# Performance work log

Measured on AMD Instinct MI355X. Metric: run time of the kernel, lower is better.

The kernel has to match this reference:

```python
import jax, jax.numpy as jnp
import numpy as np
import math

B, L, DIM, H = 1, 2048, 512, 8
D = DIM // H
STEPS = 1024
TWO_PI = 2.0 * math.pi
CHUNK = 64  # matches torch chunk_size


def setup_inputs() -> dict:
    key = jax.random.key(0)
    ks = jax.random.split(key, 6)
    x = jax.random.normal(ks[0], (B, L, DIM), jnp.float32)
    W_qs = jax.random.normal(ks[1], (DIM, 2 * DIM), jnp.float32) * 0.02
    b_qs = jnp.zeros((2 * DIM,), jnp.float32)
    ln_w = jnp.ones((2 * DIM,), jnp.float32)
    ln_b = jnp.zeros((2 * DIM,), jnp.float32)
    freq = jax.random.normal(ks[2], (H,), jnp.float32) * 0.02
    phase_shift = jax.random.normal(ks[3], (H,), jnp.float32) * 0.02
    W_out = jax.random.normal(ks[4], (DIM, DIM), jnp.float32) * 0.02
    b_out = jnp.zeros((DIM,), jnp.float32)
    # buffer: cos(linspace(0, 2pi, 1024)) exactly as in _init_lookup_tables
    cos_table = jnp.cos(jnp.linspace(0.0, TWO_PI, STEPS)).astype(jnp.float32)
    return dict(x=x, W_qs=W_qs, b_qs=b_qs, ln_w=ln_w, ln_b=ln_b,
                freq=freq, phase_shift=phase_shift, W_out=W_out, b_out=b_out,
                cos_table=cos_table)


def _forward(x, W_qs, b_qs, ln_w, ln_b, freq, phase_shift, W_out, b_out, cos_table):
    # quantum state preparation (shared module applied to same x => q == k states)
    qs = x @ W_qs + b_qs                                  # [B,L,2*DIM]
    mu = jnp.mean(qs, axis=-1, keepdims=True)
    var = jnp.var(qs, axis=-1, keepdims=True)
    qs = (qs - mu) / jnp.sqrt(var + 1e-5) * ln_w + ln_b    # LayerNorm(2*dim)
    amp, phase = jnp.split(qs, 2, axis=-1)                 # [B,L,DIM] each
    amp = jax.nn.sigmoid(amp)
    amp = amp / (jnp.sqrt(jnp.sum(amp ** 2, axis=-1, keepdims=True)) + 1e-8)
    phase = jnp.tanh(phase) * math.pi

    to_heads = lambda t: t.reshape(B, L, H, D).transpose(0, 2, 1, 3)  # [B,H,L,D]
    q_amp = to_heads(amp)
    q_phase = to_heads(phase)
    v = to_heads(x)

    NC = L // CHUNK
    qa_c = q_amp.reshape(B, H, NC, CHUNK, D).transpose(2, 0, 1, 3, 4)   # [NC,B,H,C,D]
    qp_c = q_phase.reshape(B, H, NC, CHUNK, D).transpose(2, 0, 1, 3, 4)
    f = freq[None, :, None, None, None]
    s = phase_shift[None, :, None, None, None]

    def chunk(carry, qc):
        qa, qp = qc                                         # [B,H,C,D]
        # pairwise per-dim phase interference via lookup table
        pd = (qp[:, :, :, None, :] - q_phase[:, :, None, :, :]) * f + s  # [B,H,C,L,D]
        idx = ((pd / TWO_PI * STEPS) % STEPS).astype(jnp.int32)
        interf = cos_table[idx]
        score = jnp.sum(qa[:, :, :, None, :] * q_amp[:, :, None, :, :] * interf,
                        axis=-1)                            # [B,H,C,L]
        return carry, score

    _, scores = jax.lax.scan(jax.checkpoint(chunk), 0, (qa_c, qp_c))
    scores = scores.transpose(1, 2, 0, 3, 4).reshape(B, H, L, L)
    attn = jax.nn.softmax(scores / math.sqrt(D), axis=-1)
    out = jnp.einsum('bhqk,bhkd->bhqd', attn, v)            # [B,H,L,D]
    out = out.transpose(0, 2, 1, 3).reshape(B, L, DIM)
    return out @ W_out + b_out


def reference(x, W_qs, b_qs, ln_w, ln_b, freq, phase_shift, W_out, b_out, cos_table):
    return _forward(x, W_qs, b_qs, ln_w, ln_b, freq, phase_shift, W_out, b_out, cos_table)
```

## Files before the change

### kernel.cpp

```cpp
#include <hip/hip_runtime.h>
#include <cstdint>
#include <cstddef>


typedef __attribute__((ext_vector_type(8))) short short8;
typedef __attribute__((ext_vector_type(4))) float f32x4;

#define MFMA16(a, b, c) __builtin_amdgcn_mfma_f32_16x16x32_bf16((a), (b), (c), 0, 0, 0)

static constexpr size_t B_ATTB = 0;
static constexpr size_t B_UB   = (size_t)2 * 1024 * 1024;
static constexpr size_t B_WB   = B_UB + (size_t)4 * 1024 * 1024;
static constexpr size_t B_VT   = B_WB + (size_t)4 * 1024 * 1024;
static constexpr size_t B_WQT  = B_VT + (size_t)2 * 1024 * 1024;
static constexpr size_t B_WOT  = B_WQT + (size_t)1 * 1024 * 1024;

__device__ __forceinline__ unsigned short f2bf(float f) {
  unsigned u = __float_as_uint(f);
  return (unsigned short)((u + 0x7FFFu + ((u >> 16) & 1u)) >> 16);
}

__global__ __launch_bounds__(256) void k_prep(const float* __restrict__ x,
    const float* __restrict__ Wq, const float* __restrict__ Wo,
    unsigned short* __restrict__ vT, unsigned short* __restrict__ WqTp,
    unsigned short* __restrict__ WoT) {
  __shared__ float tl[64 * 65];
  const int t = threadIdx.x, b = blockIdx.x;
  if (b < 256) {
    const int i0 = (b >> 3) * 64, h = b & 7;
    #pragma unroll
    for (int it = 0; it < 16; ++it) {
      int n = t + 256 * it;
      int r = n >> 6, c = n & 63;
      tl[r * 65 + c] = x[(size_t)(i0 + r) * 512 + h * 64 + c];
    }
    __syncthreads();
    #pragma unroll
    for (int it = 0; it < 16; ++it) {
      int n = t + 256 * it;
      int d = n >> 6, ii = n & 63;
      vT[(size_t)(h * 64 + d) * 2048 + i0 + ii] = f2bf(tl[ii * 65 + d]);
    }
  } else if (b < 384) {
    const int bb = b - 256;
    const int k0 = (bb >> 4) * 64, n0 = (bb & 15) * 64;
    #pragma unroll
    for (int it = 0; it < 16; ++it) {
      int n = t + 256 * it;
      int r = n >> 6, c = n & 63;
      tl[r * 65 + c] = Wq[(size_t)(k0 + r) * 1024 + n0 + c];
    }
    __syncthreads();
    #pragma unroll
    for (int it = 0; it < 16; ++it) {
      int n = t + 256 * it;
      int rr = n >> 6, cc = n & 63;
      int nn = n0 + rr, kk = k0 + cc;
      int nt = nn >> 4, mm = nn & 15;
      int kc32 = kk >> 5, qd = (kk >> 3) & 3, j = kk & 7;
      WqTp[(((size_t)nt * 16 + kc32) * 64 + qd * 16 + mm) * 8 + j] =
          f2bf(tl[cc * 65 + rr]);
    }
  } else {
    const int bb = b - 384;
    const int k0 = (bb >> 3) * 64, n0 = (bb & 7) * 64;
    #pragma unroll
    for (int it = 0; it < 16; ++it) {
      int n = t + 256 * it;
      int r = n >> 6, c = n & 63;
      tl[r * 65 + c] = Wo[(size_t)(k0 + r) * 512 + n0 + c];
    }
    __syncthreads();
    #pragma unroll
    for (int it = 0; it < 16; ++it) {
      int n = t + 256 * it;
      int rr = n >> 6, cc = n & 63;
      WoT[(size_t)(n0 + rr) * 512 + k0 + cc] = f2bf(tl[cc * 65 + rr]);
    }
  }
}

__global__ __launch_bounds__(512) void k_qs_ln(const float* __restrict__ x,
    const unsigned short* __restrict__ WqTp, const float* __restrict__ bq,
    const float* __restrict__ lnw, const float* __restrict__ lnb,
    const float* __restrict__ fr, const float* __restrict__ psh,
    unsigned short* __restrict__ Ub, unsigned short* __restrict__ Wb) {
  __shared__ __align__(16) unsigned short s_a[16 * 520];
  __shared__ float s_amp[16 * 516];
  __shared__ float red[8 * 16 * 2];
  __shared__ float red2[4 * 16];
  const int r0 = blockIdx.x * 16, t = threadIdx.x;
  const int w = t >> 6, lane = t & 63, m = lane & 15, quad = lane >> 4;
  {
    const int row = t >> 5, cs = (t & 31) * 16;
    const float4* xr = (const float4*)(x + (size_t)(r0 + row) * 512 + cs);
    unsigned short tmp[16];
    #pragma unroll
    for (int q4 = 0; q4 < 4; ++q4) {
      float4 v = xr[q4];
      tmp[q4 * 4 + 0] = f2bf(v.x); tmp[q4 * 4 + 1] = f2bf(v.y);
      tmp[q4 * 4 + 2] = f2bf(v.z); tmp[q4 * 4 + 3] = f2bf(v.w);
    }
    *(short8*)(s_a + row * 520 + cs)     = *(short8*)(tmp);
    *(short8*)(s_a + row * 520 + cs + 8) = *(short8*)(tmp + 8);
  }
  __syncthreads();
  f32x4 acc[8] = {{0,0,0,0},{0,0,0,0},{0,0,0,0},{0,0,0,0},
                  {0,0,0,0},{0,0,0,0},{0,0,0,0},{0,0,0,0}};
  for (int kc32 = 0; kc32 < 16; ++kc32) {
    short8 af = *(const short8*)(s_a + m * 520 + kc32 * 32 + quad * 8);
    const unsigned short* bp =
        WqTp + (((size_t)(w * 8) * 16 + kc32) * 64 + lane) * 8;
    #pragma unroll
    for (int nt = 0; nt < 8; ++nt) {
      short8 bf = *(const short8*)(bp + (size_t)nt * 8192);
      acc[nt] = MFMA16(af, bf, acc[nt]);
    }
  }
  #pragma unroll
  for (int nt = 0; nt < 8; ++nt) {
    float bv = bq[w * 128 + nt * 16 + m];
    #pragma unroll
    for (int r = 0; r < 4; ++r) acc[nt][r] += bv;
  }
  float s1[4] = {0, 0, 0, 0}, s2[4] = {0, 0, 0, 0};
  #pragma unroll
  for (int r = 0; r < 4; ++r)
    #pragma unroll
    for (int nt = 0; nt < 8; ++nt) {
      float v = acc[nt][r];
      s1[r] += v; s2[r] += v * v;
    }
  #pragma unroll
  for (int off = 1; off < 16; off <<= 1)
    #pragma unroll
    for (int r = 0; r < 4; ++r) {
      s1[r] += __shfl_xor(s1[r], off, 64);
      s2[r] += __shfl_xor(s2[r], off, 64);
    }
  if (m == 0)
    #pragma unroll
    for (int r = 0; r < 4; ++r) {
      red[(w * 16 + quad * 4 + r) * 2]     = s1[r];
      red[(w * 16 + quad * 4 + r) * 2 + 1] = s2[r];
    }
  __syncthreads();
  float mu[4], rstd[4];
  #pragma unroll
  for (int r = 0; r < 4; ++r) {
    int row = quad * 4 + r;
    float S = 0, S2 = 0;
    #pragma unroll
    for (int wp = 0; wp < 8; ++wp) {
      S  += red[(wp * 16 + row) * 2];
      S2 += red[(wp * 16 + row) * 2 + 1];
    }
    mu[r] = S * (1.0f / 1024.0f);
    float var = S2 * (1.0f / 1024.0f) - mu[r] * mu[r];
    rstd[r] = 1.0f / sqrtf(var + 1e-5f);
  }
  float y[8][4];
  #pragma unroll
  for (int nt = 0; nt < 8; ++nt) {
    int c = w * 128 + nt * 16 + m;
    float gw = lnw[c], gb = lnb[c];
    #pragma unroll
    for (int r = 0; r < 4; ++r)
      y[nt][r] = (acc[nt][r] - mu[r]) * rstd[r] * gw + gb;
  }
  const float PI_F = 3.14159265358979323846f;
  if (w < 4) {
    float a[8][4];
    float na[4] = {0, 0, 0, 0};
    #pragma unroll
    for (int nt = 0; nt < 8; ++nt)
      #pragma unroll
      for (int r = 0; r < 4; ++r) {
        float v = __builtin_amdgcn_rcpf(1.0f + __expf(-y[nt][r]));
        a[nt][r] = v;
        na[r] += v * v;
      }
    #pragma unroll
    for (int off = 1; off < 16; off <<= 1)
      #pragma unroll
      for (int r = 0; r < 4; ++r) na[r] += __shfl_xor(na[r], off, 64);
    if (m == 0)
      #pragma unroll
      for (int r = 0; r < 4; ++r) red2[w * 16 + quad * 4 + r] = na[r];
    __syncthreads();
    float inv[4];
    #pragma unroll
    for (int r = 0; r < 4; ++r) {
      int row = quad * 4 + r;
      float N = red2[row] + red2[16 + row] + red2[32 + row] + red2[48 + row];
      inv[r] = 1.0f / (sqrtf(N) + 1e-8f);
    }
    #pragma unroll
    for (int nt = 0; nt < 8; ++nt)
      #pragma unroll
      for (int r = 0; r < 4; ++r)
        s_amp[(quad * 4 + r) * 516 + w * 128 + nt * 16 + m] = a[nt][r] * inv[r];
    __syncthreads();
  } else {
    float p[8][4];
    #pragma unroll
    for (int nt = 0; nt < 8; ++nt)
      #pragma unroll
      for (int r = 0; r < 4; ++r) {
        float e2 = __expf(2.0f * y[nt][r]);
        p[nt][r] = (1.0f - 2.0f * __builtin_amdgcn_rcpf(e2 + 1.0f)) * PI_F;
      }
    __syncthreads();
    __syncthreads();
    const double GAM = 1024.0 / 1023.0;
    const int hbase = (w - 4) * 2;
    float c1[2], s1g[2];
    #pragma unroll
    for (int hh = 0; hh < 2; ++hh) {
      c1[hh]  = (float)((double)fr[hbase + hh] * GAM);
      s1g[hh] = (float)((double)psh[hbase + hh] * GAM);
    }
    #pragma unroll
    for (int nt = 0; nt < 8; ++nt) {
      const int hh = nt >> 2;
      const int pc = (w - 4) * 128 + nt * 16 + m;
      const int d = pc & 63;
      #pragma unroll
      for (int r = 0; r < 4; ++r) {
        const int i = r0 + quad * 4 + r;
        float af = s_amp[(quad * 4 + r) * 516 + pc];
        float A = fmaf(p[nt][r], c1[hh], s1g[hh]);
        float Bp = p[nt][r] * c1[hh];
        float cA, sA, cB, sB;
        __sincosf(A, &sA, &cA);
        __sincosf(Bp, &sB, &cB);
        size_t base = ((size_t)(hbase + hh) * 2048 + i) * 128 + d;
        Ub[base]      = f2bf(af * cA);
        Ub[base + 64] = f2bf(af * sA);
        Wb[base]      = f2bf(af * cB);
        Wb[base + 64] = f2bf(af * sB);
      }
    }
  }
}

__global__ __launch_bounds__(512, 1) void k_flash6(const unsigned short* __restrict__ Ub,
    const unsigned short* __restrict__ Wb, const unsigned short* __restrict__ vT,
    unsigned short* __restrict__ attb) {
  __shared__ __align__(16) unsigned char s_w[2][128 * 272];
  __shared__ __align__(16) unsigned char s_v[2][64 * 272];
  __shared__ __align__(16) unsigned char s_p[2][64 * 272];
  const int qt = blockIdx.x, h = blockIdx.y;
  const int q0 = qt * 64;
  const int t = threadIdx.x;
  const int wave = t >> 6, lane = t & 63;
  const int qg = wave & 3, dh = wave >> 2;
  const int m = lane & 15, quad = lane >> 4;
  const int sr = t >> 2, sp = t & 3;
  const int vr = t >> 3, vp = t & 7;
  short8 afr[4][4];
  #pragma unroll
  for (int g = 0; g < 4; ++g) {
    const unsigned short* urow = Ub + ((size_t)h * 2048 + q0 + g * 16 + m) * 128;
    #pragma unroll
    for (int fs = 0; fs < 4; ++fs)
      afr[g][fs] = *(const short8*)(urow + fs * 32 + quad * 8);
  }
  short8 ones;
  #pragma unroll
  for (int j = 0; j < 8; ++j) ones[j] = (short)0x3F80;
  f32x4 oacc[2] = {{0,0,0,0},{0,0,0,0}};
  f32x4 dacc = {0, 0, 0, 0};
  const unsigned short* wgbase = Wb + (size_t)h * 2048 * 128 + (size_t)sr * 128;
  const unsigned short* vgbase = vT + ((size_t)h * 64 + vr) * 2048;
  #pragma unroll
  for (int it = 0; it < 4; ++it)
    *(short8*)(s_w[0] + sr * 272 + sp * 64 + it * 16) =
      *(const short8*)(wgbase + sp * 32 + it * 8);
  #pragma unroll
  for (int it = 0; it < 2; ++it)
    *(short8*)(s_v[0] + vr * 272 + vp * 32 + it * 16) =
      *(const short8*)(vgbase + vp * 16 + it * 8);
  __syncthreads();
  for (int kt = 0; kt < 16; ++kt) {
    const int cur = kt & 1;
    short8 wst[4], vst[2];
    const bool has = (kt < 15);
    if (has) {
      const unsigned short* wg = wgbase + (size_t)(kt + 1) * 128 * 128;
      #pragma unroll
      for (int it = 0; it < 4; ++it)
        wst[it] = *(const short8*)(wg + sp * 32 + it * 8);
      const unsigned short* vg = vgbase + (kt + 1) * 128;
      #pragma unroll
      for (int it = 0; it < 2; ++it)
        vst[it] = *(const short8*)(vg + vp * 16 + it * 8);
    }
    f32x4 sc[4] = {{0,0,0,0},{0,0,0,0},{0,0,0,0},{0,0,0,0}};
    #pragma unroll
    for (int fs = 0; fs < 4; ++fs) {
      short8 bfr = *(const short8*)(s_w[cur] + (wave * 16 + m) * 272 + fs * 64 + quad * 16);
      #pragma unroll
      for (int g = 0; g < 4; ++g)
        sc[g] = MFMA16(afr[g][fs], bfr, sc[g]);
    }
    #pragma unroll
    for (int g = 0; g < 4; ++g)
      #pragma unroll
      for (int r = 0; r < 4; ++r) {
        float p = __expf(sc[g][r] * 0.125f);
        *(unsigned short*)(s_p[cur] + (g * 16 + quad * 4 + r) * 272 +
                           (wave * 16 + m) * 2) = f2bf(p);
      }
    short8 vf[4][2];
    #pragma unroll
    for (int k2 = 0; k2 < 4; ++k2)
      #pragma unroll
      for (int dt = 0; dt < 2; ++dt)
        vf[k2][dt] = *(const short8*)(s_v[cur] + (dh * 32 + dt * 16 + m) * 272 +
                                      k2 * 64 + quad * 16);
    if (has) {
      #pragma unroll
      for (int it = 0; it < 4; ++it)
        *(short8*)(s_w[cur ^ 1] + sr * 272 + sp * 64 + it * 16) = wst[it];
      #pragma unroll
      for (int it = 0; it < 2; ++it)
        *(short8*)(s_v[cur ^ 1] + vr * 272 + vp * 32 + it * 16) = vst[it];
    }
    __syncthreads();
    #pragma unroll
    for (int k2 = 0; k2 < 4; ++k2) {
      short8 pf = *(const short8*)(s_p[cur] + (qg * 16 + m) * 272 + k2 * 64 + quad * 16);
      dacc = MFMA16(pf, ones, dacc);
      #pragma unroll
      for (int dt = 0; dt < 2; ++dt)
        oacc[dt] = MFMA16(pf, vf[k2][dt], oacc[dt]);
    }
  }
  float invd[4];
  #pragma unroll
  for (int r = 0; r < 4; ++r) invd[r] = 1.0f / dacc[r];
  #pragma unroll
  for (int dt = 0; dt < 2; ++dt)
    #pragma unroll
    for (int r = 0; r < 4; ++r)
      attb[(size_t)(q0 + qg * 16 + quad * 4 + r) * 512 + h * 64 +
           dh * 32 + dt * 16 + m] = f2bf(oacc[dt][r] * invd[r]);
}

__global__ __launch_bounds__(256) void k_gemm(const unsigned short* __restrict__ A,
    const unsigned short* __restrict__ Bt, const float* __restrict__ bias,
    float* __restrict__ C, int N) {
  __shared__ __align__(16) unsigned char sm[2 * 64 * 136];
  unsigned char* s_a = sm;
  unsigned char* s_b = sm + 64 * 136;
  const int m0 = blockIdx.x * 64, n0 = blockIdx.y * 64;
  const int t = threadIdx.x;
  const int wave = t >> 6, lane = t & 63;
  const int m = lane & 15, quad = lane >> 4;
  const int sr = t >> 2, spart = t & 3;
  f32x4 acc[4] = {{0,0,0,0},{0,0,0,0},{0,0,0,0},{0,0,0,0}};
  for (int kc = 0; kc < 512; kc += 64) {
    #pragma unroll
    for (int it = 0; it < 2; ++it) {
      *(short8*)(s_a + sr * 136 + spart * 32 + it * 16) =
        *(const short8*)(A + (size_t)(m0 + sr) * 512 + kc + spart * 16 + it * 8);
      *(short8*)(s_b + sr * 136 + spart * 32 + it * 16) =
        *(const short8*)(Bt + (size_t)(n0 + sr) * 512 + kc + spart * 16 + it * 8);
    }
    __syncthreads();
    #pragma unroll
    for (int k2 = 0; k2 < 2; ++k2) {
      short8 af = *(const short8*)(s_a + (wave * 16 + m) * 136 + k2 * 64 + quad * 16);
      #pragma unroll
      for (int nt = 0; nt < 4; ++nt) {
        short8 bf = *(const short8*)(s_b + (nt * 16 + m) * 136 + k2 * 64 + quad * 16);
        acc[nt] = MFMA16(af, bf, acc[nt]);
      }
    }
    __syncthreads();
  }
  #pragma unroll
  for (int nt = 0; nt < 4; ++nt) {
    int col = n0 + nt * 16 + m;
    float bv = bias[col];
    #pragma unroll
    for (int r = 0; r < 4; ++r) {
      int row = m0 + wave * 16 + quad * 4 + r;
      C[(size_t)row * N + col] = acc[nt][r] + bv;
    }
  }
}

extern "C" void kernel_launch(void* const* d_in, const int* in_sizes, int n_in,
                              void* d_out, int out_size, void* d_ws, size_t ws_size,
                              hipStream_t stream) {
  (void)in_sizes; (void)n_in; (void)out_size; (void)ws_size;
  const float* x   = (const float*)d_in[0];
  const float* Wq  = (const float*)d_in[1];
  const float* bq  = (const float*)d_in[2];
  const float* lnw = (const float*)d_in[3];
  const float* lnb = (const float*)d_in[4];
  const float* fr  = (const float*)d_in[5];
  const float* ps  = (const float*)d_in[6];
  const float* Wo  = (const float*)d_in[7];
  const float* bo  = (const float*)d_in[8];
  char* ws = (char*)d_ws;
  unsigned short* attb = (unsigned short*)(ws + B_ATTB);
  unsigned short* Ub   = (unsigned short*)(ws + B_UB);
  unsigned short* Wb   = (unsigned short*)(ws + B_WB);
  unsigned short* vT   = (unsigned short*)(ws + B_VT);
  unsigned short* WqTp = (unsigned short*)(ws + B_WQT);
  unsigned short* WoT  = (unsigned short*)(ws + B_WOT);
  float* out = (float*)d_out;

  k_prep<<<448, 256, 0, stream>>>(x, Wq, Wo, vT, WqTp, WoT);
  k_qs_ln<<<128, 512, 0, stream>>>(x, WqTp, bq, lnw, lnb, fr, ps, Ub, Wb);
  k_flash6<<<dim3(32, 8), 512, 0, stream>>>(Ub, Wb, vT, attb);
  k_gemm<<<dim3(32, 8), 256, 0, stream>>>(attb, WoT, bo, out, 512);
}
```

Baseline: 147.5 us.

## Double-buffer Wq tiles through LDS with register prefetch in QS+LayerNorm GEMM

The QS projection GEMM now stages weight fragments in a 2x64KB LDS double buffer instead of reading them straight from global memory inside the MFMA loop. Each iteration prefetches the next k-slice into registers while the MFMAs consume the current buffer, then writes the prefetch into the other buffer and synchronises the block. The s_amp scratch is aliased onto the first buffer, and the launch bounds now ask for 2 blocks per CU. The large LDS footprint and the per-iteration block barrier are the cost, and there is no cross-wave reuse of the weights to gain from staging.

After: 142.3 us. -3.5%, faster.

```diff
diff --git a/kernel.cpp b/kernel.cpp
--- a/kernel.cpp
+++ b/kernel.cpp
@@ -80,15 +80,16 @@
   }
 }
 
-__global__ __launch_bounds__(512) void k_qs_ln(const float* __restrict__ x,
+__global__ __launch_bounds__(512, 2) void k_qs_ln(const float* __restrict__ x,
     const unsigned short* __restrict__ WqTp, const float* __restrict__ bq,
     const float* __restrict__ lnw, const float* __restrict__ lnb,
     const float* __restrict__ fr, const float* __restrict__ psh,
     unsigned short* __restrict__ Ub, unsigned short* __restrict__ Wb) {
+  __shared__ __align__(16) unsigned char s_bb[2][65536];
   __shared__ __align__(16) unsigned short s_a[16 * 520];
-  __shared__ float s_amp[16 * 516];
   __shared__ float red[8 * 16 * 2];
   __shared__ float red2[4 * 16];
+  float* s_amp = (float*)(&s_bb[0][0]);
   const int r0 = blockIdx.x * 16, t = threadIdx.x;
   const int w = t >> 6, lane = t & 63, m = lane & 15, quad = lane >> 4;
   {
@@ -104,18 +105,36 @@
     *(short8*)(s_a + row * 520 + cs)     = *(short8*)(tmp);
     *(short8*)(s_a + row * 520 + cs + 8) = *(short8*)(tmp + 8);
   }
+  const unsigned short* gB = WqTp + (size_t)w * 8192 + (size_t)lane * 8;
+  #pragma unroll
+  for (int it = 0; it < 8; ++it)
+    *(short8*)(s_bb[0] + (it * 8 + w) * 1024 + lane * 16) =
+        *(const short8*)(gB + (size_t)it * 65536);
   __syncthreads();
   f32x4 acc[8] = {{0,0,0,0},{0,0,0,0},{0,0,0,0},{0,0,0,0},
                   {0,0,0,0},{0,0,0,0},{0,0,0,0},{0,0,0,0}};
-  for (int kc32 = 0; kc32 < 16; ++kc32) {
-    short8 af = *(const short8*)(s_a + m * 520 + kc32 * 32 + quad * 8);
-    const unsigned short* bp =
-        WqTp + (((size_t)(w * 8) * 16 + kc32) * 64 + lane) * 8;
+  for (int kc = 0; kc < 16; ++kc) {
+    const int cur = kc & 1;
+    short8 st[8];
+    const bool has = (kc < 15);
+    if (has) {
+      const unsigned short* g = gB + (size_t)(kc + 1) * 512;
+      #pragma unroll
+      for (int it = 0; it < 8; ++it)
+        st[it] = *(const short8*)(g + (size_t)it * 65536);
+    }
+    short8 af = *(const short8*)(s_a + m * 520 + kc * 32 + quad * 8);
     #pragma unroll
     for (int nt = 0; nt < 8; ++nt) {
-      short8 bf = *(const short8*)(bp + (size_t)nt * 8192);
+      short8 bf = *(const short8*)(s_bb[cur] + (w * 8 + nt) * 1024 + lane * 16);
       acc[nt] = MFMA16(af, bf, acc[nt]);
     }
+    if (has) {
+      #pragma unroll
+      for (int it = 0; it < 8; ++it)
+        *(short8*)(s_bb[cur ^ 1] + (it * 8 + w) * 1024 + lane * 16) = st[it];
+    }
+    __syncthreads();
   }
   #pragma unroll
   for (int nt = 0; nt < 8; ++nt) {
```

## Split fused QS GEMM+LayerNorm kernel into wide GEMM and per-row LN/feature kernels

Applied to the files above, without the earlier changes.

The single 128-block kernel that did the x@W_qs GEMM, LayerNorm, sigmoid/tanh and feature generation is replaced by two kernels. The first is a 2048-block GEMM that writes fp32 qs plus per-tile partial sums. The second is a 2048-block per-row kernel that finishes the LayerNorm statistics and produces the Ub/Wb features with packed stores. The goal is to fill the GPU better, since 128 blocks leave most CUs idle. The cost is an extra kernel launch and an fp32 round trip of the qs intermediate through global memory.

Measured after the change: 140.2 us. 4.9% less time.

```diff
diff --git a/kernel.cpp b/kernel.cpp
--- a/kernel.cpp
+++ b/kernel.cpp
@@ -14,6 +14,8 @@
 static constexpr size_t B_VT   = B_WB + (size_t)4 * 1024 * 1024;
 static constexpr size_t B_WQT  = B_VT + (size_t)2 * 1024 * 1024;
 static constexpr size_t B_WOT  = B_WQT + (size_t)1 * 1024 * 1024;
+static constexpr size_t B_QS   = (size_t)14 * 1024 * 1024;
+static constexpr size_t B_PST  = (size_t)23 * 1024 * 1024;
 
 __device__ __forceinline__ unsigned short f2bf(float f) {
   unsigned u = __float_as_uint(f);
@@ -80,57 +82,46 @@
   }
 }
 
-__global__ __launch_bounds__(512) void k_qs_ln(const float* __restrict__ x,
+__global__ __launch_bounds__(256) void k_qs_gemm(const float* __restrict__ x,
     const unsigned short* __restrict__ WqTp, const float* __restrict__ bq,
-    const float* __restrict__ lnw, const float* __restrict__ lnb,
-    const float* __restrict__ fr, const float* __restrict__ psh,
-    unsigned short* __restrict__ Ub, unsigned short* __restrict__ Wb) {
+    float* __restrict__ qs, float* __restrict__ pst) {
   __shared__ __align__(16) unsigned short s_a[16 * 520];
-  __shared__ float s_amp[16 * 516];
-  __shared__ float red[8 * 16 * 2];
-  __shared__ float red2[4 * 16];
-  const int r0 = blockIdx.x * 16, t = threadIdx.x;
+  __shared__ float s_q[16 * 68];
+  const int t = threadIdx.x;
+  const int rt = blockIdx.x >> 4, cg = blockIdx.x & 15;
   const int w = t >> 6, lane = t & 63, m = lane & 15, quad = lane >> 4;
+  const int ct = cg * 4 + w;
   {
-    const int row = t >> 5, cs = (t & 31) * 16;
-    const float4* xr = (const float4*)(x + (size_t)(r0 + row) * 512 + cs);
-    unsigned short tmp[16];
-    #pragma unroll
-    for (int q4 = 0; q4 < 4; ++q4) {
+    const int row = t >> 4, cs = (t & 15) * 32;
+    const float4* xr = (const float4*)(x + (size_t)(rt * 16 + row) * 512 + cs);
+    unsigned short tmp[32];
+    #pragma unroll
+    for (int q4 = 0; q4 < 8; ++q4) {
       float4 v = xr[q4];
       tmp[q4 * 4 + 0] = f2bf(v.x); tmp[q4 * 4 + 1] = f2bf(v.y);
       tmp[q4 * 4 + 2] = f2bf(v.z); tmp[q4 * 4 + 3] = f2bf(v.w);
     }
-    *(short8*)(s_a + row * 520 + cs)     = *(short8*)(tmp);
-    *(short8*)(s_a + row * 520 + cs + 8) = *(short8*)(tmp + 8);
-  }
-  __syncthreads();
-  f32x4 acc[8] = {{0,0,0,0},{0,0,0,0},{0,0,0,0},{0,0,0,0},
-                  {0,0,0,0},{0,0,0,0},{0,0,0,0},{0,0,0,0}};
-  for (int kc32 = 0; kc32 < 16; ++kc32) {
-    short8 af = *(const short8*)(s_a + m * 520 + kc32 * 32 + quad * 8);
-    const unsigned short* bp =
-        WqTp + (((size_t)(w * 8) * 16 + kc32) * 64 + lane) * 8;
-    #pragma unroll
-    for (int nt = 0; nt < 8; ++nt) {
-      short8 bf = *(const short8*)(bp + (size_t)nt * 8192);
-      acc[nt] = MFMA16(af, bf, acc[nt]);
-    }
-  }
-  #pragma unroll
-  for (int nt = 0; nt < 8; ++nt) {
-    float bv = bq[w * 128 + nt * 16 + m];
-    #pragma unroll
-    for (int r = 0; r < 4; ++r) acc[nt][r] += bv;
-  }
-  float s1[4] = {0, 0, 0, 0}, s2[4] = {0, 0, 0, 0};
-  #pragma unroll
-  for (int r = 0; r < 4; ++r)
-    #pragma unroll
-    for (int nt = 0; nt < 8; ++nt) {
-      float v = acc[nt][r];
-      s1[r] += v; s2[r] += v * v;
-    }
+    #pragma unroll
+    for (int q8 = 0; q8 < 4; ++q8)
+      *(short8*)(s_a + row * 520 + cs + q8 * 8) = *(short8*)(tmp + q8 * 8);
+  }
+  __syncthreads();
+  f32x4 acc = {0, 0, 0, 0};
+  const unsigned short* bp = WqTp + ((size_t)ct * 16 * 64 + lane) * 8;
+  #pragma unroll
+  for (int kc = 0; kc < 16; ++kc) {
+    short8 af = *(const short8*)(s_a + m * 520 + kc * 32 + quad * 8);
+    short8 bf = *(const short8*)(bp + (size_t)kc * 512);
+    acc = MFMA16(af, bf, acc);
+  }
+  {
+    float bv = bq[ct * 16 + m];
+    #pragma unroll
+    for (int r = 0; r < 4; ++r) acc[r] += bv;
+  }
+  float s1[4], s2[4];
+  #pragma unroll
+  for (int r = 0; r < 4; ++r) { s1[r] = acc[r]; s2[r] = acc[r] * acc[r]; }
   #pragma unroll
   for (int off = 1; off < 16; off <<= 1)
     #pragma unroll
@@ -141,107 +132,81 @@
   if (m == 0)
     #pragma unroll
     for (int r = 0; r < 4; ++r) {
-      red[(w * 16 + quad * 4 + r) * 2]     = s1[r];
-      red[(w * 16 + quad * 4 + r) * 2 + 1] = s2[r];
-    }
-  __syncthreads();
-  float mu[4], rstd[4];
-  #pragma unroll
-  for (int r = 0; r < 4; ++r) {
-    int row = quad * 4 + r;
-    float S = 0, S2 = 0;
-    #pragma unroll
-    for (int wp = 0; wp < 8; ++wp) {
-      S  += red[(wp * 16 + row) * 2];
-      S2 += red[(wp * 16 + row) * 2 + 1];
-    }
-    mu[r] = S * (1.0f / 1024.0f);
-    float var = S2 * (1.0f / 1024.0f) - mu[r] * mu[r];
-    rstd[r] = 1.0f / sqrtf(var + 1e-5f);
-  }
-  float y[8][4];
-  #pragma unroll
-  for (int nt = 0; nt < 8; ++nt) {
-    int c = w * 128 + nt * 16 + m;
-    float gw = lnw[c], gb = lnb[c];
-    #pragma unroll
-    for (int r = 0; r < 4; ++r)
-      y[nt][r] = (acc[nt][r] - mu[r]) * rstd[r] * gw + gb;
-  }
+      float2 pv = {s1[r], s2[r]};
+      *(float2*)(pst + ((size_t)(rt * 16 + quad * 4 + r) * 64 + ct) * 2) = pv;
+    }
+  #pragma unroll
+  for (int r = 0; r < 4; ++r)
+    s_q[(quad * 4 + r) * 68 + w * 16 + m] = acc[r];
+  __syncthreads();
+  {
+    const int row = t >> 4, c4 = (t & 15) * 4;
+    float4 v = *(const float4*)(s_q + row * 68 + c4);
+    *(float4*)(qs + (size_t)(rt * 16 + row) * 1024 + cg * 64 + c4) = v;
+  }
+}
+
+__global__ __launch_bounds__(256) void k_ln_feat(const float* __restrict__ qs,
+    const float* __restrict__ pst, const float* __restrict__ lnw,
+    const float* __restrict__ lnb, const float* __restrict__ fr,
+    const float* __restrict__ psh, unsigned short* __restrict__ Ub,
+    unsigned short* __restrict__ Wb) {
+  __shared__ float bc[2];
+  __shared__ float rna[4];
+  const int row = blockIdx.x, t = threadIdx.x;
+  const int w = t >> 6, lane = t & 63;
+  if (w == 0) {
+    float2 p = *(const float2*)(pst + ((size_t)row * 64 + lane) * 2);
+    float S = p.x, S2 = p.y;
+    #pragma unroll
+    for (int off = 1; off < 64; off <<= 1) {
+      S  += __shfl_xor(S, off, 64);
+      S2 += __shfl_xor(S2, off, 64);
+    }
+    if (lane == 0) { bc[0] = S; bc[1] = S2; }
+  }
+  __syncthreads();
+  const float mu = bc[0] * (1.0f / 1024.0f);
+  const float var = bc[1] * (1.0f / 1024.0f) - mu * mu;
+  const float rstd = 1.0f / sqrtf(var + 1e-5f);
+  const int pc = t * 2;
+  float2 qa = *(const float2*)(qs + (size_t)row * 1024 + pc);
+  float2 qp = *(const float2*)(qs + (size_t)row * 1024 + 512 + pc);
+  const float ya0 = (qa.x - mu) * rstd * lnw[pc]     + lnb[pc];
+  const float ya1 = (qa.y - mu) * rstd * lnw[pc + 1] + lnb[pc + 1];
+  const float yp0 = (qp.x - mu) * rstd * lnw[512 + pc]     + lnb[512 + pc];
+  const float yp1 = (qp.y - mu) * rstd * lnw[512 + pc + 1] + lnb[512 + pc + 1];
+  const float a0 = __builtin_amdgcn_rcpf(1.0f + __expf(-ya0));
+  const float a1 = __builtin_amdgcn_rcpf(1.0f + __expf(-ya1));
+  float na = a0 * a0 + a1 * a1;
+  #pragma unroll
+  for (int off = 1; off < 64; off <<= 1) na += __shfl_xor(na, off, 64);
+  if (lane == 0) rna[w] = na;
+  __syncthreads();
+  const float N = rna[0] + rna[1] + rna[2] + rna[3];
+  const float inv = 1.0f / (sqrtf(N) + 1e-8f);
   const float PI_F = 3.14159265358979323846f;
-  if (w < 4) {
-    float a[8][4];
-    float na[4] = {0, 0, 0, 0};
-    #pragma unroll
-    for (int nt = 0; nt < 8; ++nt)
-      #pragma unroll
-      for (int r = 0; r < 4; ++r) {
-        float v = __builtin_amdgcn_rcpf(1.0f + __expf(-y[nt][r]));
-        a[nt][r] = v;
-        na[r] += v * v;
-      }
-    #pragma unroll
-    for (int off = 1; off < 16; off <<= 1)
-      #pragma unroll
-      for (int r = 0; r < 4; ++r) na[r] += __shfl_xor(na[r], off, 64);
-    if (m == 0)
-      #pragma unroll
-      for (int r = 0; r < 4; ++r) red2[w * 16 + quad * 4 + r] = na[r];
-    __syncthreads();
-    float inv[4];
-    #pragma unroll
-    for (int r = 0; r < 4; ++r) {
-      int row = quad * 4 + r;
-      float N = red2[row] + red2[16 + row] + red2[32 + row] + red2[48 + row];
-      inv[r] = 1.0f / (sqrtf(N) + 1e-8f);
-    }
-    #pragma unroll
-    for (int nt = 0; nt < 8; ++nt)
-      #pragma unroll
-      for (int r = 0; r < 4; ++r)
-        s_amp[(quad * 4 + r) * 516 + w * 128 + nt * 16 + m] = a[nt][r] * inv[r];
-    __syncthreads();
-  } else {
-    float p[8][4];
-    #pragma unroll
-    for (int nt = 0; nt < 8; ++nt)
-      #pragma unroll
-      for (int r = 0; r < 4; ++r) {
-        float e2 = __expf(2.0f * y[nt][r]);
-        p[nt][r] = (1.0f - 2.0f * __builtin_amdgcn_rcpf(e2 + 1.0f)) * PI_F;
-      }
-    __syncthreads();
-    __syncthreads();
-    const double GAM = 1024.0 / 1023.0;
-    const int hbase = (w - 4) * 2;
-    float c1[2], s1g[2];
-    #pragma unroll
-    for (int hh = 0; hh < 2; ++hh) {
-      c1[hh]  = (float)((double)fr[hbase + hh] * GAM);
-      s1g[hh] = (float)((double)psh[hbase + hh] * GAM);
-    }
-    #pragma unroll
-    for (int nt = 0; nt < 8; ++nt) {
-      const int hh = nt >> 2;
-      const int pc = (w - 4) * 128 + nt * 16 + m;
-      const int d = pc & 63;
-      #pragma unroll
-      for (int r = 0; r < 4; ++r) {
-        const int i = r0 + quad * 4 + r;
-        float af = s_amp[(quad * 4 + r) * 516 + pc];
-        float A = fmaf(p[nt][r], c1[hh], s1g[hh]);
-        float Bp = p[nt][r] * c1[hh];
-        float cA, sA, cB, sB;
-        __sincosf(A, &sA, &cA);
-        __sincosf(Bp, &sB, &cB);
-        size_t base = ((size_t)(hbase + hh) * 2048 + i) * 128 + d;
-        Ub[base]      = f2bf(af * cA);
-        Ub[base + 64] = f2bf(af * sA);
-        Wb[base]      = f2bf(af * cB);
-        Wb[base + 64] = f2bf(af * sB);
-      }
-    }
-  }
+  const float e20 = __expf(2.0f * yp0);
+  const float e21 = __expf(2.0f * yp1);
+  const float p0 = (1.0f - 2.0f * __builtin_amdgcn_rcpf(e20 + 1.0f)) * PI_F;
+  const float p1 = (1.0f - 2.0f * __builtin_amdgcn_rcpf(e21 + 1.0f)) * PI_F;
+  const double GAM = 1024.0 / 1023.0;
+  const int h = pc >> 6, d = pc & 63;
+  const float c1  = (float)((double)fr[h]  * GAM);
+  const float s1g = (float)((double)psh[h] * GAM);
+  const float af0 = a0 * inv, af1 = a1 * inv;
+  const float A0 = fmaf(p0, c1, s1g), B0 = p0 * c1;
+  const float A1 = fmaf(p1, c1, s1g), B1 = p1 * c1;
+  float cA0, sA0, cB0, sB0, cA1, sA1, cB1, sB1;
+  __sincosf(A0, &sA0, &cA0);
+  __sincosf(B0, &sB0, &cB0);
+  __sincosf(A1, &sA1, &cA1);
+  __sincosf(B1, &sB1, &cB1);
+  const size_t base = ((size_t)h * 2048 + row) * 128 + d;
+  *(unsigned*)(Ub + base)      = (unsigned)f2bf(af0 * cA0) | ((unsigned)f2bf(af1 * cA1) << 16);
+  *(unsigned*)(Ub + base + 64) = (unsigned)f2bf(af0 * sA0) | ((unsigned)f2bf(af1 * sA1) << 16);
+  *(unsigned*)(Wb + base)      = (unsigned)f2bf(af0 * cB0) | ((unsigned)f2bf(af1 * cB1) << 16);
+  *(unsigned*)(Wb + base + 64) = (unsigned)f2bf(af0 * sB0) | ((unsigned)f2bf(af1 * sB1) << 16);
 }
 
 __global__ __launch_bounds__(512, 1) void k_flash6(const unsigned short* __restrict__ Ub,
@@ -412,10 +377,13 @@
   unsigned short* vT   = (unsigned short*)(ws + B_VT);
   unsigned short* WqTp = (unsigned short*)(ws + B_WQT);
   unsigned short* WoT  = (unsigned short*)(ws + B_WOT);
+  float* qs  = (float*)(ws + B_QS);
+  float* pst = (float*)(ws + B_PST);
   float* out = (float*)d_out;
 
   k_prep<<<448, 256, 0, stream>>>(x, Wq, Wo, vT, WqTp, WoT);
-  k_qs_ln<<<128, 512, 0, stream>>>(x, WqTp, bq, lnw, lnb, fr, ps, Ub, Wb);
+  k_qs_gemm<<<2048, 256, 0, stream>>>(x, WqTp, bq, qs, pst);
+  k_ln_feat<<<2048, 256, 0, stream>>>(qs, pst, lnw, lnb, fr, ps, Ub, Wb);
   k_flash6<<<dim3(32, 8), 512, 0, stream>>>(Ub, Wb, vT, attb);
   k_gemm<<<dim3(32, 8), 256, 0, stream>>>(attb, WoT, bo, out, 512);
 }
```
